# Performance work log

Measured on AMD Instinct MI355X. Metric: run time of the kernel, lower is better.

## Reference

```python
import jax, jax.numpy as jnp
import numpy as np

B, N, E, D, H, L = 1024, 64, 1024, 128, 4, 2
C = D // H          # per-head out_channels
K = 5               # options per attribute
LN_EPS = 1e-5


def setup_inputs() -> dict:
    key = jax.random.key(0)
    ks = jax.random.split(key, 22)
    s = 0.05
    inp = {
        'x': jax.random.randint(ks[0], (B, N), 0, K),
        'edge_index': jax.random.randint(ks[1], (2, E), 0, N),
        'edge_attr': jax.random.uniform(ks[2], (E, 1), jnp.float32),
        # tokenizer params
        'attr_emb': jax.random.normal(ks[3], (N, D), jnp.float32) * s,
        'opt_emb': jax.random.normal(ks[4], (N, K, D), jnp.float32) * s,
        'prior': jnp.ones((N, 1), jnp.float32),
        # GATv2 params, stacked over layers
        'Wl': jax.random.normal(ks[5], (L, D, D), jnp.float32) * s,
        'bl': jnp.zeros((L, D), jnp.float32),
        'Wr': jax.random.normal(ks[6], (L, D, D), jnp.float32) * s,
        'br': jnp.zeros((L, D), jnp.float32),
        'We': jax.random.normal(ks[7], (L, 1, D), jnp.float32) * s,
        'att': jax.random.normal(ks[8], (L, H, C), jnp.float32) * s,
        'conv_bias': jnp.zeros((L, D), jnp.float32),
        'ln_g': jnp.ones((L, D), jnp.float32),
        'ln_b': jnp.zeros((L, D), jnp.float32),
        # reliability head
        'W1': jax.random.normal(ks[9], (2 * D, D), jnp.float32) * s,
        'b1': jnp.zeros((D,), jnp.float32),
        'W2': jax.random.normal(ks[10], (D, 1), jnp.float32) * s,
        'b2': jnp.zeros((1,), jnp.float32),
    }
    return inp


def _forward(x, edge_index, edge_attr, attr_emb, opt_emb, prior,
             Wl, bl, Wr, br, We, att, conv_bias, ln_g, ln_b, W1, b1, W2, b2):
    Bb, n = x.shape
    # Tokenizer: token_i = p_i * (E_attr[i] + E_val[i](x_i))
    val = opt_emb[jnp.arange(n)[None, :], x]                 # [B,n,D]
    T0 = (attr_emb[None] + val) * prior[None]                # [B,n,D]

    src, dst = edge_index[0], edge_index[1]
    h = T0
    for l in range(Wl.shape[0]):
        xl = (h @ Wl[l] + bl[l]).reshape(Bb, n, H, C)        # source transform
        xr = (h @ Wr[l] + br[l]).reshape(Bb, n, H, C)        # target transform
        e = (edge_attr @ We[l]).reshape(1, E, H, C)          # edge embedding
        msg = xl[:, src]                                     # [B,E,H,C]
        z = jax.nn.leaky_relu(msg + xr[:, dst] + e, 0.2)
        alpha = jnp.einsum('behc,hc->beh', z, att[l])        # [B,E,H]
        # segment softmax over incoming edges per target node
        mx = jnp.full((Bb, n, H), -jnp.inf, alpha.dtype).at[:, dst].max(alpha)
        ex = jnp.exp(alpha - mx[:, dst])
        den = jnp.zeros((Bb, n, H), alpha.dtype).at[:, dst].add(ex)
        a = ex / den[:, dst]                                 # normalized attention
        out = jnp.zeros((Bb, n, H, C), h.dtype).at[:, dst].add(msg * a[..., None])
        g = out.reshape(Bb, n, D) + conv_bias[l]
        mu = g.mean(-1, keepdims=True)
        var = g.var(-1, keepdims=True)
        g = (g - mu) / jnp.sqrt(var + LN_EPS) * ln_g[l] + ln_b[l]
        g = jax.nn.elu(g)
        h = h + g                                            # residual

    hat_T = jnp.concatenate([T0, h], axis=-1)                # [B,n,2D]
    rel = jax.nn.sigmoid(jax.nn.relu(hat_T @ W1 + b1) @ W2 + b2)[..., 0]  # [B,n]
    rw = rel[..., None]
    f_scale = (h * rw).sum(1) / (rw.sum(1) + 1e-8)           # [B,D]
    return f_scale, rel, hat_T


def reference(x, edge_index, edge_attr, attr_emb, opt_emb, prior,
              Wl, bl, Wr, br, We, att, conv_bias, ln_g, ln_b, W1, b1, W2, b2):
    return _forward(x, edge_index, edge_attr, attr_emb, opt_emb, prior,
                    Wl, bl, Wr, br, We, att, conv_bias, ln_g, ln_b, W1, b1, W2, b2)
```

## Files before the change

kernel.cpp:

```cpp
#include <hip/hip_runtime.h>
#include <hip/hip_bf16.h>

#define Bv 1024
#define Nv 64
#define Ev 1024
#define Dv 128
#define Hv 4
#define Lv 2
#define Kv 5
#define PAD 130

typedef __hip_bfloat16 bf16;
typedef __attribute__((ext_vector_type(8))) short bf16x8_t;
typedef __attribute__((ext_vector_type(4))) float f32x4_t;
typedef __attribute__((ext_vector_type(2))) float f32x2_t;

__device__ __forceinline__ float b2f(bf16 v) { return __bfloat162float(v); }
__device__ __forceinline__ bf16  f2b(float v) { return __float2bfloat16(v); }

__device__ bf16 g_pWl[(size_t)Lv * 2 * Dv * Dv];
__device__ bf16 g_pWr[(size_t)Lv * 2 * Dv * Dv];
__device__ bf16 g_pW1[(size_t)2 * 2 * Dv * Dv];
__device__ float g_K[Lv * Hv];
__device__ unsigned int g_etab[Ev];
__device__ int          g_off[Nv + 1];

__device__ __forceinline__ f32x2_t unpack2v(unsigned int u) {
    union { unsigned int u; float f; } a, b;
    a.u = u << 16;
    b.u = u & 0xffff0000u;
    return (f32x2_t){a.f, b.f};
}

__device__ __forceinline__ unsigned int pack2v(f32x2_t v) {
    union { bf16 b; unsigned short u; } lo, hi;
    lo.b = f2b(v.x); hi.b = f2b(v.y);
    return (unsigned int)lo.u | ((unsigned int)hi.u << 16);
}

__device__ __forceinline__ bf16x8_t load_a_frag(const bf16* buf, int elem_idx) {
    const unsigned int* p = (const unsigned int*)buf;
    union { bf16x8_t v; unsigned int u[4]; } r;
    int d = elem_idx >> 1;
    r.u[0] = p[d]; r.u[1] = p[d + 1]; r.u[2] = p[d + 2]; r.u[3] = p[d + 3];
    return r.v;
}

__device__ void pack_mat(const float* __restrict__ W, bf16* __restrict__ out,
                         int K, int tid, int nth)
{
    const int total = K * 128;
    for (int e = tid; e < total; e += nth) {
        int f    = e >> 9;
        int rem  = e & 511;
        int lane = rem >> 3;
        int i    = rem & 7;
        int kk   = f >> 3;
        int nt   = f & 7;
        int col  = nt * 16 + (lane & 15);
        int k    = kk * 32 + (lane >> 4) * 8 + i;
        float w  = W[k * 128 + col];
        bf16 hi  = f2b(w);
        out[e]         = hi;
        out[total + e] = f2b(w - b2f(hi));
    }
}

__global__ void prep(const int* __restrict__ edge_index, const float* __restrict__ edge_attr,
                     const float* __restrict__ Wl, const float* __restrict__ Wr,
                     const float* __restrict__ W1, const float* __restrict__ We,
                     const float* __restrict__ att)
{
    const int bid = blockIdx.x;
    if (bid == 0) {
        __shared__ int cnt[Nv];
        int tid = threadIdx.x;
        if (tid < Nv) cnt[tid] = 0;
        __syncthreads();
        for (int e = tid; e < Ev; e += blockDim.x)
            atomicAdd(&cnt[edge_index[Ev + e]], 1);
        __syncthreads();
        if (tid == 0) {
            int s = 0;
            for (int t = 0; t < Nv; ++t) { int c = cnt[t]; g_off[t] = s; cnt[t] = s; s += c; }
            g_off[Nv] = s;
        }
        __syncthreads();
        for (int e = tid; e < Ev; e += blockDim.x) {
            int s = edge_index[e];
            int d = edge_index[Ev + e];
            int pos = atomicAdd(&cnt[d], 1);
            union { bf16 b; unsigned short u; } cv;
            cv.b = f2b(edge_attr[e]);
            g_etab[pos] = (unsigned int)(s | (d << 6)) | ((unsigned int)cv.u << 16);
        }
        return;
    }
    const int nth = (gridDim.x - 1) * 256;
    const int tid = (bid - 1) * 256 + threadIdx.x;
    for (int l = 0; l < Lv; ++l) {
        pack_mat(Wl + (size_t)l * Dv * Dv, g_pWl + (size_t)l * 2 * Dv * Dv, Dv, tid, nth);
        pack_mat(Wr + (size_t)l * Dv * Dv, g_pWr + (size_t)l * 2 * Dv * Dv, Dv, tid, nth);
    }
    pack_mat(W1, g_pW1, 2 * Dv, tid, nth);
    if (bid == 1 && threadIdx.x < Lv * Hv) {
        int l = threadIdx.x / Hv, h = threadIdx.x % Hv;
        float k = 0.f;
        for (int c = 0; c < 32; ++c)
            k += att[l * Dv + h * 32 + c] * We[l * Dv + h * 32 + c];
        g_K[threadIdx.x] = 0.2f * k;
    }
}

__global__ __launch_bounds__(512, 2)
void gat_fused(const int* __restrict__ x,
               const float* __restrict__ attr_emb,
               const float* __restrict__ opt_emb, const float* __restrict__ prior,
               const float* __restrict__ bl, const float* __restrict__ br,
               const float* __restrict__ conv_bias, const float* __restrict__ ln_g,
               const float* __restrict__ ln_b,
               const float* __restrict__ b1, const float* __restrict__ W2,
               const float* __restrict__ b2,
               const float* __restrict__ We, const float* __restrict__ att,
               float* __restrict__ out_fscale, float* __restrict__ out_rel,
               float* __restrict__ out_hatT)
{
    const int b = blockIdx.x;
    const int tid = threadIdx.x;

    __shared__ __align__(16) bf16 hs [Nv * PAD];
    __shared__ __align__(16) bf16 xls[Nv * PAD];
    __shared__ __align__(16) bf16 xrs[Nv * PAD];
    __shared__ bf16 alphas[Ev * Hv];
    __shared__ __align__(16) float red [Nv * 8];
    __shared__ __align__(16) float red2[Nv * 8];
    __shared__ __align__(16) float wecol[Dv];
    __shared__ __align__(16) float attv [Dv];
    __shared__ float relbuf[Nv];

    const int my_t  = tid & 63;
    const int beg   = g_off[my_t];
    const int end   = g_off[my_t + 1];

    for (int idx = tid; idx < Nv * Dv; idx += 512) {
        int n = idx >> 7, d = idx & 127;
        float t0 = (attr_emb[n * Dv + d] + opt_emb[(n * Kv + x[b * Nv + n]) * Dv + d])
                   * prior[n];
        hs[n * PAD + d] = f2b(t0);
    }

    for (int l = 0; l < Lv; ++l) {
        if (tid < Dv) {
            wecol[tid] = We[l * Dv + tid];
            attv[tid]  = att[l * Dv + tid];
        }
        __syncthreads();

        {
            const int w = tid >> 6, lane = tid & 63;
            const int row16 = lane & 15, kg = lane >> 4;
            const bf16* pB = (w < 4) ? (g_pWl + (size_t)l * 2 * Dv * Dv)
                                     : (g_pWr + (size_t)l * 2 * Dv * Dv);
            const int wc = (w & 3) * 32;
            bf16* dst = (w < 4) ? xls : xrs;
            const float* bias = (w < 4) ? (bl + l * Dv) : (br + l * Dv);

            #pragma unroll
            for (int nt = 0; nt < 2; ++nt) {
                f32x4_t acc[4];
                #pragma unroll
                for (int mt = 0; mt < 4; ++mt)
                    acc[mt] = (f32x4_t){0.f, 0.f, 0.f, 0.f};

                #pragma unroll
                for (int kk = 0; kk < 4; ++kk) {
                    const int kb = kk * 32 + kg * 8;
                    const int f = kk * 8 + (w & 3) * 2 + nt;
                    bf16x8_t bh  = *(const bf16x8_t*)&pB[(size_t)(f * 64 + lane) * 8];
                    bf16x8_t blo = *(const bf16x8_t*)&pB[Dv * Dv + (size_t)(f * 64 + lane) * 8];
                    #pragma unroll
                    for (int mt = 0; mt < 4; ++mt) {
                        bf16x8_t a = load_a_frag(hs, (mt * 16 + row16) * PAD + kb);
                        acc[mt] = __builtin_amdgcn_mfma_f32_16x16x32_bf16(a, bh,  acc[mt], 0, 0, 0);
                        acc[mt] = __builtin_amdgcn_mfma_f32_16x16x32_bf16(a, blo, acc[mt], 0, 0, 0);
                    }
                }
                const int col = wc + nt * 16 + row16;
                const float bv = bias[col];
                #pragma unroll
                for (int mt = 0; mt < 4; ++mt) {
                    #pragma unroll
                    for (int r = 0; r < 4; ++r) {
                        const int row = mt * 16 + kg * 4 + r;
                        dst[row * PAD + col] = f2b(acc[mt][r] + bv);
                    }
                }
            }
        }
        __syncthreads();

        {
            const int t = tid & 63, h = (tid >> 6) & 3, half = tid >> 8;
            const int ch0 = h * 32 + half * 16;
            f32x2_t dl2 = {0.f, 0.f};
            #pragma unroll
            for (int c = 0; c < 16; c += 2) {
                f32x2_t a2 = *(const f32x2_t*)&attv[ch0 + c];
                dl2 += a2 * unpack2v(*(const unsigned int*)&xls[t * PAD + ch0 + c]);
            }
            red[t * 8 + h * 2 + half] = dl2.x + dl2.y;
        }
        __syncthreads();

        {
            const int h = (tid >> 6) & 3, half = tid >> 8, lane = tid & 63;
            const float k02 = g_K[l * Hv + h];
            const f32x2_t zero2 = {0.f, 0.f};
            for (int it = 0; it < 8; ++it) {
                int pos = (half * 8 + it) * 64 + lane;
                unsigned int et = g_etab[pos];
                int s = et & 63, t = (et >> 6) & 63;
                union { unsigned int u; float f; } ec; ec.u = et & 0xffff0000u;
                float ea = ec.f;
                f32x2_t ea2 = {ea, ea};
                f32x2_t acc2 = {0.f, 0.f};
                int bs = s * PAD + h * 32, bt = t * PAD + h * 32;
                #pragma unroll
                for (int c = 0; c < 32; c += 2) {
                    f32x2_t xl2 = unpack2v(*(const unsigned int*)&xls[bs + c]);
                    f32x2_t xr2 = unpack2v(*(const unsigned int*)&xrs[bt + c]);
                    f32x2_t we2 = *(const f32x2_t*)&wecol[h * 32 + c];
                    f32x2_t at2 = *(const f32x2_t*)&attv [h * 32 + c];
                    f32x2_t v   = xl2 + xr2 + ea2 * we2;
                    acc2 += at2 * __builtin_elementwise_max(v, zero2);
                }
                float dL = red[s * 8 + h * 2] + red[s * 8 + h * 2 + 1];
                float alpha = 0.2f * dL + k02 * ea + 0.8f * (acc2.x + acc2.y);
                alphas[pos * Hv + h] = f2b(alpha);
            }
        }
        __syncthreads();

        {
            const int t = my_t, h = (tid >> 6) & 3, half = tid >> 8;
            const int ch0 = h * 32 + half * 16;
            float mx = -3e38f;
            for (int idx = beg; idx < end; ++idx)
                mx = fmaxf(mx, b2f(alphas[idx * Hv + h]));
            f32x2_t acc2[8];
            #pragma unroll
            for (int j = 0; j < 8; ++j) acc2[j] = (f32x2_t){0.f, 0.f};
            float den = 0.f;
            for (int idx = beg; idx < end; ++idx) {
                int s = (int)(g_etab[idx] & 63u);
                float ex = expf(b2f(alphas[idx * Hv + h]) - mx);
                den += ex;
                f32x2_t ex2 = {ex, ex};
                int bs = s * PAD + ch0;
                #pragma unroll
                for (int j = 0; j < 8; ++j)
                    acc2[j] += ex2 * unpack2v(*(const unsigned int*)&xls[bs + 2 * j]);
            }
            float inv_den = (end > beg) ? 1.f / den : 0.f;
            f32x2_t id2 = {inv_den, inv_den};
            f32x2_t sum2 = {0.f, 0.f}, sq2 = {0.f, 0.f};
            #pragma unroll
            for (int j = 0; j < 8; ++j) {
                f32x2_t cb = *(const f32x2_t*)&conv_bias[l * Dv + ch0 + 2 * j];
                f32x2_t g  = acc2[j] * id2 + cb;
                acc2[j] = g;
                sum2 += g; sq2 += g * g;
            }
            red [t * 8 + h * 2 + half] = sum2.x + sum2.y;
            red2[t * 8 + h * 2 + half] = sq2.x + sq2.y;
            __syncthreads();
            float mu = 0.f, ms = 0.f;
            #pragma unroll
            for (int j = 0; j < 8; ++j) { mu += red[t * 8 + j]; ms += red2[t * 8 + j]; }
            mu *= (1.f / 128.f); ms *= (1.f / 128.f);
            float rstd = rsqrtf(ms - mu * mu + 1e-5f);
            f32x2_t mu2 = {mu, mu}, rs2 = {rstd, rstd};
            #pragma unroll
            for (int j = 0; j < 8; ++j) {
                f32x2_t lg = *(const f32x2_t*)&ln_g[l * Dv + ch0 + 2 * j];
                f32x2_t lb = *(const f32x2_t*)&ln_b[l * Dv + ch0 + 2 * j];
                f32x2_t g  = (acc2[j] - mu2) * rs2 * lg + lb;
                g.x = g.x > 0.f ? g.x : (expf(g.x) - 1.f);
                g.y = g.y > 0.f ? g.y : (expf(g.y) - 1.f);
                unsigned int* hp = (unsigned int*)&hs[t * PAD + ch0 + 2 * j];
                f32x2_t hv = unpack2v(*hp) + g;
                *hp = pack2v(hv);
            }
        }
        __syncthreads();
    }

    if (tid < Dv) wecol[tid] = W2[tid];
    for (int idx = tid; idx < Nv * Dv; idx += 512) {
        int n = idx >> 7, d = idx & 127;
        float t0 = (attr_emb[n * Dv + d] + opt_emb[(n * Kv + x[b * Nv + n]) * Dv + d])
                   * prior[n];
        xrs[n * PAD + d] = f2b(t0);
        size_t rb = ((size_t)(b * Nv + n)) * (2 * Dv);
        out_hatT[rb + d]      = t0;
        out_hatT[rb + Dv + d] = b2f(hs[n * PAD + d]);
    }
    __syncthreads();

    {
        const int w = tid >> 6, lane = tid & 63;
        const int row16 = lane & 15, kg = lane >> 4;
        f32x4_t acc[4];
        #pragma unroll
        for (int mt = 0; mt < 4; ++mt)
            acc[mt] = (f32x4_t){0.f, 0.f, 0.f, 0.f};

        #pragma unroll
        for (int kk = 0; kk < 8; ++kk) {
            const bf16* asrc = (kk < 4) ? xrs : hs;
            const int kb = (kk & 3) * 32 + kg * 8;
            const int f = kk * 8 + w;
            bf16x8_t bh  = *(const bf16x8_t*)&g_pW1[(size_t)(f * 64 + lane) * 8];
            bf16x8_t blo = *(const bf16x8_t*)&g_pW1[(size_t)2 * Dv * Dv + (size_t)(f * 64 + lane) * 8];
            #pragma unroll
            for (int mt = 0; mt < 4; ++mt) {
                bf16x8_t a = load_a_frag(asrc, (mt * 16 + row16) * PAD + kb);
                acc[mt] = __builtin_amdgcn_mfma_f32_16x16x32_bf16(a, bh,  acc[mt], 0, 0, 0);
                acc[mt] = __builtin_amdgcn_mfma_f32_16x16x32_bf16(a, blo, acc[mt], 0, 0, 0);
            }
        }
        #pragma unroll
        for (int mt = 0; mt < 4; ++mt) {
            const int col = w * 16 + row16;
            #pragma unroll
            for (int r = 0; r < 4; ++r) {
                const int row = mt * 16 + kg * 4 + r;
                float v = acc[mt][r] + b1[col];
                xls[row * PAD + col] = f2b(v > 0.f ? v : 0.f);
            }
        }
    }
    __syncthreads();

    {
        const int t = tid & 63, h = (tid >> 6) & 3, half = tid >> 8;
        const int ch0 = h * 32 + half * 16;
        f32x2_t s2 = {0.f, 0.f};
        #pragma unroll
        for (int c = 0; c < 16; c += 2) {
            f32x2_t h2 = unpack2v(*(const unsigned int*)&xls[t * PAD + ch0 + c]);
            s2 += h2 * *(const f32x2_t*)&wecol[ch0 + c];
        }
        red[t * 8 + h * 2 + half] = s2.x + s2.y;
        __syncthreads();
        if (h == 0 && half == 0) {
            float z = b2[0];
            #pragma unroll
            for (int j = 0; j < 8; ++j) z += red[t * 8 + j];
            float r = 1.f / (1.f + expf(-z));
            relbuf[t] = r;
            out_rel[b * Nv + t] = r;
        }
    }
    __syncthreads();

    if (tid < Dv) {
        float num = 0.f, den = 0.f;
        for (int n = 0; n < Nv; ++n) {
            float r = relbuf[n];
            num += b2f(hs[n * PAD + tid]) * r;
            den += r;
        }
        out_fscale[b * Dv + tid] = num / (den + 1e-8f);
    }
}

extern "C" void kernel_launch(void* const* d_in, const int* in_sizes, int n_in,
                              void* d_out, int out_size, void* d_ws, size_t ws_size,
                              hipStream_t stream)
{
    const int*   x          = (const int*)  d_in[0];
    const int*   edge_index = (const int*)  d_in[1];
    const float* edge_attr  = (const float*)d_in[2];
    const float* attr_emb   = (const float*)d_in[3];
    const float* opt_emb    = (const float*)d_in[4];
    const float* prior      = (const float*)d_in[5];
    const float* Wl         = (const float*)d_in[6];
    const float* bl         = (const float*)d_in[7];
    const float* Wr         = (const float*)d_in[8];
    const float* br         = (const float*)d_in[9];
    const float* We         = (const float*)d_in[10];
    const float* att        = (const float*)d_in[11];
    const float* conv_bias  = (const float*)d_in[12];
    const float* ln_g       = (const float*)d_in[13];
    const float* ln_b       = (const float*)d_in[14];
    const float* W1         = (const float*)d_in[15];
    const float* b1         = (const float*)d_in[16];
    const float* W2         = (const float*)d_in[17];
    const float* b2         = (const float*)d_in[18];

    float* out        = (float*)d_out;
    float* out_fscale = out;
    float* out_rel    = out + (size_t)Bv * Dv;
    float* out_hatT   = out + (size_t)Bv * Dv + (size_t)Bv * Nv;

    prep<<<129, 256, 0, stream>>>(edge_index, edge_attr, Wl, Wr, W1, We, att);
    gat_fused<<<Bv, 512, 0, stream>>>(x, attr_emb, opt_emb,
                                      prior, bl, br, conv_bias,
                                      ln_g, ln_b, b1, W2, b2, We, att,
                                      out_fscale, out_rel, out_hatT);
}
```

Before: 293.3 us.

## Use 16-byte LDS loads with PAD 136 and interleaved We/att table

Row padding grows from 130 to 136 bf16 so every 8-element fragment is 16-byte aligned. Scattered 4-byte LDS reads then become single 128-bit loads in the MFMA A-fragments, the attention dot products, the edge scoring and the aggregation. We and att are interleaved into one float table so a single f32x4 load gives both, and the edge loop is reorganised to process 8 edges per thread across 4 channel chunks. The wider padding may change LDS bank-conflict patterns, and the larger unrolled edge loop raises register pressure.

```diff
diff --git a/kernel.cpp b/kernel.cpp
--- a/kernel.cpp
+++ b/kernel.cpp
@@ -8,7 +8,7 @@
 #define Hv 4
 #define Lv 2
 #define Kv 5
-#define PAD 130
+#define PAD 136
 
 typedef __hip_bfloat16 bf16;
 typedef __attribute__((ext_vector_type(8))) short bf16x8_t;
@@ -38,13 +38,10 @@
     return (unsigned int)lo.u | ((unsigned int)hi.u << 16);
 }
 
-__device__ __forceinline__ bf16x8_t load_a_frag(const bf16* buf, int elem_idx) {
-    const unsigned int* p = (const unsigned int*)buf;
-    union { bf16x8_t v; unsigned int u[4]; } r;
-    int d = elem_idx >> 1;
-    r.u[0] = p[d]; r.u[1] = p[d + 1]; r.u[2] = p[d + 2]; r.u[3] = p[d + 3];
-    return r.v;
-}
+__device__ __forceinline__ bf16x8_t load8(const bf16* p, int elem) {
+    return *(const bf16x8_t*)(p + elem);
+}
+union b8u { bf16x8_t v; unsigned int u[4]; };
 
 __device__ void pack_mat(const float* __restrict__ W, bf16* __restrict__ out,
                          int K, int tid, int nth)
@@ -131,11 +128,11 @@
     __shared__ __align__(16) bf16 hs [Nv * PAD];
     __shared__ __align__(16) bf16 xls[Nv * PAD];
     __shared__ __align__(16) bf16 xrs[Nv * PAD];
-    __shared__ bf16 alphas[Ev * Hv];
+    __shared__ __align__(16) bf16 alphas[Ev * Hv];
     __shared__ __align__(16) float red [Nv * 8];
     __shared__ __align__(16) float red2[Nv * 8];
-    __shared__ __align__(16) float wecol[Dv];
-    __shared__ __align__(16) float attv [Dv];
+    __shared__ __align__(16) float watt[256];
+    __shared__ __align__(16) float w2col[Dv];
     __shared__ float relbuf[Nv];
 
     const int my_t  = tid & 63;
@@ -150,9 +147,10 @@
     }
 
     for (int l = 0; l < Lv; ++l) {
-        if (tid < Dv) {
-            wecol[tid] = We[l * Dv + tid];
-            attv[tid]  = att[l * Dv + tid];
+        if (tid < 256) {
+            int h = tid >> 6, cp = (tid >> 2) & 15, e = tid & 3;
+            int c = cp * 2 + (e & 1);
+            watt[tid] = (e < 2) ? We[l * Dv + h * 32 + c] : att[l * Dv + h * 32 + c];
         }
         __syncthreads();
 
@@ -180,7 +178,7 @@
                     bf16x8_t blo = *(const bf16x8_t*)&pB[Dv * Dv + (size_t)(f * 64 + lane) * 8];
                     #pragma unroll
                     for (int mt = 0; mt < 4; ++mt) {
-                        bf16x8_t a = load_a_frag(hs, (mt * 16 + row16) * PAD + kb);
+                        bf16x8_t a = load8(hs, (mt * 16 + row16) * PAD + kb);
                         acc[mt] = __builtin_amdgcn_mfma_f32_16x16x32_bf16(a, bh,  acc[mt], 0, 0, 0);
                         acc[mt] = __builtin_amdgcn_mfma_f32_16x16x32_bf16(a, blo, acc[mt], 0, 0, 0);
                     }
@@ -202,11 +200,19 @@
         {
             const int t = tid & 63, h = (tid >> 6) & 3, half = tid >> 8;
             const int ch0 = h * 32 + half * 16;
+            b8u a0, a1;
+            a0.v = load8(xls, t * PAD + ch0);
+            a1.v = load8(xls, t * PAD + ch0 + 8);
             f32x2_t dl2 = {0.f, 0.f};
             #pragma unroll
-            for (int c = 0; c < 16; c += 2) {
-                f32x2_t a2 = *(const f32x2_t*)&attv[ch0 + c];
-                dl2 += a2 * unpack2v(*(const unsigned int*)&xls[t * PAD + ch0 + c]);
+            for (int j = 0; j < 4; ++j) {
+                f32x2_t at2 = *(const f32x2_t*)&watt[h * 64 + (half * 8 + j) * 4 + 2];
+                dl2 += at2 * unpack2v(a0.u[j]);
+            }
+            #pragma unroll
+            for (int j = 0; j < 4; ++j) {
+                f32x2_t at2 = *(const f32x2_t*)&watt[h * 64 + (half * 8 + 4 + j) * 4 + 2];
+                dl2 += at2 * unpack2v(a1.u[j]);
             }
             red[t * 8 + h * 2 + half] = dl2.x + dl2.y;
         }
@@ -216,27 +222,46 @@
             const int h = (tid >> 6) & 3, half = tid >> 8, lane = tid & 63;
             const float k02 = g_K[l * Hv + h];
             const f32x2_t zero2 = {0.f, 0.f};
-            for (int it = 0; it < 8; ++it) {
-                int pos = (half * 8 + it) * 64 + lane;
-                unsigned int et = g_etab[pos];
-                int s = et & 63, t = (et >> 6) & 63;
-                union { unsigned int u; float f; } ec; ec.u = et & 0xffff0000u;
-                float ea = ec.f;
-                f32x2_t ea2 = {ea, ea};
-                f32x2_t acc2 = {0.f, 0.f};
-                int bs = s * PAD + h * 32, bt = t * PAD + h * 32;
-                #pragma unroll
-                for (int c = 0; c < 32; c += 2) {
-                    f32x2_t xl2 = unpack2v(*(const unsigned int*)&xls[bs + c]);
-                    f32x2_t xr2 = unpack2v(*(const unsigned int*)&xrs[bt + c]);
-                    f32x2_t we2 = *(const f32x2_t*)&wecol[h * 32 + c];
-                    f32x2_t at2 = *(const f32x2_t*)&attv [h * 32 + c];
-                    f32x2_t v   = xl2 + xr2 + ea2 * we2;
-                    acc2 += at2 * __builtin_elementwise_max(v, zero2);
+            unsigned int ets[8];
+            #pragma unroll
+            for (int e = 0; e < 8; ++e)
+                ets[e] = g_etab[(half * 8 + e) * 64 + lane];
+            f32x2_t acc[8];
+            #pragma unroll
+            for (int e = 0; e < 8; ++e) acc[e] = (f32x2_t){0.f, 0.f};
+
+            #pragma unroll
+            for (int q = 0; q < 4; ++q) {
+                f32x4_t wa[4];
+                #pragma unroll
+                for (int j = 0; j < 4; ++j)
+                    wa[j] = *(const f32x4_t*)&watt[h * 64 + (q * 4 + j) * 4];
+                #pragma unroll
+                for (int e = 0; e < 8; ++e) {
+                    int s = ets[e] & 63, t = (ets[e] >> 6) & 63;
+                    b8u xl, xr;
+                    xl.v = load8(xls, s * PAD + h * 32 + q * 8);
+                    xr.v = load8(xrs, t * PAD + h * 32 + q * 8);
+                    union { unsigned int u; float f; } ec; ec.u = ets[e] & 0xffff0000u;
+                    f32x2_t ea2 = {ec.f, ec.f};
+                    #pragma unroll
+                    for (int j = 0; j < 4; ++j) {
+                        f32x2_t xl2 = unpack2v(xl.u[j]);
+                        f32x2_t xr2 = unpack2v(xr.u[j]);
+                        f32x2_t we2 = {wa[j].x, wa[j].y};
+                        f32x2_t at2 = {wa[j].z, wa[j].w};
+                        f32x2_t v   = xl2 + xr2 + ea2 * we2;
+                        acc[e] += at2 * __builtin_elementwise_max(v, zero2);
+                    }
                 }
+            }
+            #pragma unroll
+            for (int e = 0; e < 8; ++e) {
+                int s = ets[e] & 63;
+                union { unsigned int u; float f; } ec; ec.u = ets[e] & 0xffff0000u;
                 float dL = red[s * 8 + h * 2] + red[s * 8 + h * 2 + 1];
-                float alpha = 0.2f * dL + k02 * ea + 0.8f * (acc2.x + acc2.y);
-                alphas[pos * Hv + h] = f2b(alpha);
+                float alpha = 0.2f * dL + k02 * ec.f + 0.8f * (acc[e].x + acc[e].y);
+                alphas[((half * 8 + e) * 64 + lane) * Hv + h] = f2b(alpha);
             }
         }
         __syncthreads();
@@ -256,10 +281,15 @@
                 float ex = expf(b2f(alphas[idx * Hv + h]) - mx);
                 den += ex;
                 f32x2_t ex2 = {ex, ex};
-                int bs = s * PAD + ch0;
-                #pragma unroll
-                for (int j = 0; j < 8; ++j)
-                    acc2[j] += ex2 * unpack2v(*(const unsigned int*)&xls[bs + 2 * j]);
+                b8u m0, m1;
+                m0.v = load8(xls, s * PAD + ch0);
+                m1.v = load8(xls, s * PAD + ch0 + 8);
+                #pragma unroll
+                for (int j = 0; j < 4; ++j)
+                    acc2[j] += ex2 * unpack2v(m0.u[j]);
+                #pragma unroll
+                for (int j = 0; j < 4; ++j)
+                    acc2[4 + j] += ex2 * unpack2v(m1.u[j]);
             }
             float inv_den = (end > beg) ? 1.f / den : 0.f;
             f32x2_t id2 = {inv_den, inv_den};
@@ -295,7 +325,7 @@
         __syncthreads();
     }
 
-    if (tid < Dv) wecol[tid] = W2[tid];
+    if (tid < Dv) w2col[tid] = W2[tid];
     for (int idx = tid; idx < Nv * Dv; idx += 512) {
         int n = idx >> 7, d = idx & 127;
         float t0 = (attr_emb[n * Dv + d] + opt_emb[(n * Kv + x[b * Nv + n]) * Dv + d])
@@ -324,7 +354,7 @@
             bf16x8_t blo = *(const bf16x8_t*)&g_pW1[(size_t)2 * Dv * Dv + (size_t)(f * 64 + lane) * 8];
             #pragma unroll
             for (int mt = 0; mt < 4; ++mt) {
-                bf16x8_t a = load_a_frag(asrc, (mt * 16 + row16) * PAD + kb);
+                bf16x8_t a = load8(asrc, (mt * 16 + row16) * PAD + kb);
                 acc[mt] = __builtin_amdgcn_mfma_f32_16x16x32_bf16(a, bh,  acc[mt], 0, 0, 0);
                 acc[mt] = __builtin_amdgcn_mfma_f32_16x16x32_bf16(a, blo, acc[mt], 0, 0, 0);
             }
@@ -345,12 +375,16 @@
     {
         const int t = tid & 63, h = (tid >> 6) & 3, half = tid >> 8;
         const int ch0 = h * 32 + half * 16;
+        b8u h0, h1;
+        h0.v = load8(xls, t * PAD + ch0);
+        h1.v = load8(xls, t * PAD + ch0 + 8);
         f32x2_t s2 = {0.f, 0.f};
         #pragma unroll
-        for (int c = 0; c < 16; c += 2) {
-            f32x2_t h2 = unpack2v(*(const unsigned int*)&xls[t * PAD + ch0 + c]);
-            s2 += h2 * *(const f32x2_t*)&wecol[ch0 + c];
-        }
+        for (int j = 0; j < 4; ++j)
+            s2 += unpack2v(h0.u[j]) * *(const f32x2_t*)&w2col[ch0 + 2 * j];
+        #pragma unroll
+        for (int j = 0; j < 4; ++j)
+            s2 += unpack2v(h1.u[j]) * *(const f32x2_t*)&w2col[ch0 + 8 + 2 * j];
         red[t * 8 + h * 2 + half] = s2.x + s2.y;
         __syncthreads();
         if (h == 0 && half == 0) {
```

After: 279.5 us. -4.7%, faster.
